# Optimization experiments

Hardware: AMD Instinct MI355X
Metric: run time of the kernel (lower is better)

Reference implementation:

```python
import jax, jax.numpy as jnp
import numpy as np

B, L, S, D, H, M, DFF, CO = 16, 512, 1024, 512, 8, 64, 2048, 512
KS = (3, 5, 7)  # MOEDecomp kernel sizes


def _avgpool(x, k):
    # AvgPool1d(kernel=k, stride=1, padding=k//2, count_include_pad=True) along L of [B,L,D]
    p = k // 2
    s = jax.lax.reduce_window(x, 0.0, jax.lax.add, (1, k, 1), (1, 1, 1), ((0, 0), (p, p), (0, 0)))
    return s / k


def _moe_decomp(x, w1, b1, w2, b2):
    trends = jnp.stack([_avgpool(x, k) for k in KS], axis=-1)          # [B,L,D,E]
    g = jax.nn.softmax(jax.nn.relu(x @ w1.T + b1) @ w2.T + b2, axis=-1)  # [B,L,E]
    trend = jnp.einsum('blde,ble->bld', trends, g)
    return x - trend, trend


def _fourier_block(x, wr, wi):
    b, l, d = x.shape
    qft = jnp.fft.rfft(x, axis=1)                                      # [B, L//2+1, D] complex
    m = min(M, qft.shape[1])
    W = wr[:, :, :m] + 1j * wi[:, :, :m]                               # [D,D,m] complex
    om = jnp.einsum('bmd,dem->bme', qft[:, :m], W)                     # per-mode complex matmul
    out_ft = jnp.zeros((b, l // 2 + 1, d), jnp.complex64).at[:, :m].set(om)
    return jnp.fft.irfft(out_ft, n=l, axis=1)


def _fourier_cross(q_in, kv, wq, bq, wk, bk, wv, bv, wo, bo):
    b, l, _ = q_in.shape
    s = kv.shape[1]
    dk = D // H
    q = (q_in @ wq.T + bq).reshape(b, l, H, dk).transpose(0, 2, 1, 3)   # [B,H,L,dk]
    k = (kv @ wk.T + bk).reshape(b, s, H, dk).transpose(0, 2, 1, 3)
    v = (kv @ wv.T + bv).reshape(b, s, H, dk).transpose(0, 2, 1, 3)
    qf = jnp.fft.rfft(q, axis=2)
    kf = jnp.fft.rfft(k, axis=2)
    vf = jnp.fft.rfft(v, axis=2)
    mq = min(M, qf.shape[2])
    mk = min(M, kf.shape[2])
    qf, kf, vf = qf[:, :, :mq], kf[:, :, :mk], vf[:, :, :mk]
    attn = (jnp.einsum('bhld,bhsd->bhls', qf.real, kf.real)
            + jnp.einsum('bhld,bhsd->bhls', qf.imag, kf.imag))
    attn = jax.nn.softmax(attn, axis=-1)
    of = jax.lax.complex(jnp.einsum('bhls,bhsd->bhld', attn, vf.real),
                         jnp.einsum('bhls,bhsd->bhld', attn, vf.imag))
    full = jnp.zeros((b, H, l // 2 + 1, dk), jnp.complex64).at[:, :, :mq].set(of)
    out = jnp.fft.irfft(full, n=l, axis=2)                              # [B,H,L,dk]
    out = out.transpose(0, 2, 1, 3).reshape(b, l, D)
    return out @ wo.T + bo


def _circ_conv(t, w):
    # Conv1d(k=3, padding=1, circular, no bias); t: [B,L,D], w: [CO,D,3]
    xt = t.transpose(0, 2, 1)                                           # [B,D,L]
    xp = jnp.concatenate([xt[:, :, -1:], xt, xt[:, :, :1]], axis=-1)
    y = jax.lax.conv_general_dilated(xp, w, (1,), 'VALID',
                                     dimension_numbers=('NCH', 'OIH', 'NCH'))
    return y.transpose(0, 2, 1)                                         # [B,L,CO]


def setup_inputs() -> dict:
    key = jax.random.key(0)
    ks = jax.random.split(key, 32)
    def n(i, shape, scale=0.02):
        return (scale * jax.random.normal(ks[i], shape)).astype(jnp.float32)
    feb_scale = 1.0 / (D * D)
    inp = {
        'x': n(0, (B, L, D), 1.0),
        'cross': n(1, (B, S, D), 1.0),
        'feb_wr': n(2, (D, D, M), feb_scale),
        'feb_wi': n(3, (D, D, M), feb_scale),
        'wq': n(4, (D, D)), 'bq': n(5, (D,)),
        'wk': n(6, (D, D)), 'bk': n(7, (D,)),
        'wv': n(8, (D, D)), 'bv': n(9, (D,)),
        'wo': n(10, (D, D)), 'bo': n(11, (D,)),
        'w_ff1': n(12, (DFF, D)), 'w_ff2': n(13, (D, DFF)),
        'd1_w1': n(14, (D // 2, D)), 'd1_b1': n(15, (D // 2,)),
        'd1_w2': n(16, (3, D // 2)), 'd1_b2': n(17, (3,)),
        'd2_w1': n(18, (D // 2, D)), 'd2_b1': n(19, (D // 2,)),
        'd2_w2': n(20, (3, D // 2)), 'd2_b2': n(21, (3,)),
        'd3_w1': n(22, (D // 2, D)), 'd3_b1': n(23, (D // 2,)),
        'd3_w2': n(24, (3, D // 2)), 'd3_b2': n(25, (3,)),
        'p1': n(26, (CO, D, 3)), 'p2': n(27, (CO, D, 3)), 'p3': n(28, (CO, D, 3)),
    }
    return inp


def reference(x, cross, feb_wr, feb_wi, wq, bq, wk, bk, wv, bv, wo, bo,
              w_ff1, w_ff2, d1_w1, d1_b1, d1_w2, d1_b2,
              d2_w1, d2_b1, d2_w2, d2_b2, d3_w1, d3_b1, d3_w2, d3_b2,
              p1, p2, p3):
    # dropout is identity (eval mode)
    x = x + _fourier_block(x, feb_wr, feb_wi)
    x, t1 = _moe_decomp(x, d1_w1, d1_b1, d1_w2, d1_b2)
    x = x + _fourier_cross(x, cross, wq, bq, wk, bk, wv, bv, wo, bo)
    x, t2 = _moe_decomp(x, d2_w1, d2_b1, d2_w2, d2_b2)
    y = jax.nn.relu(x @ w_ff1.T) @ w_ff2.T  # 1x1 convs == pointwise GEMMs
    x, t3 = _moe_decomp(x + y, d3_w1, d3_b1, d3_w2, d3_b2)
    residual_trend = _circ_conv(t1, p1) + _circ_conv(t2, p2) + _circ_conv(t3, p3)
    return x, residual_trend
```

## Files before the change

### kernel.cpp

```cpp
#include <hip/hip_runtime.h>
#include <math.h>

typedef unsigned short u16;
typedef unsigned int u32;
typedef unsigned long long u64;

constexpr int kB = 16, kL = 512, kS = 1024, kD = 512, kM = 64;

typedef __attribute__((ext_vector_type(8))) short u16x8;
typedef __attribute__((ext_vector_type(8))) _Float16 f16x8;
typedef __attribute__((ext_vector_type(4))) float f32x4;

__device__ __forceinline__ u16 f2h(float f) {
    _Float16 h = (_Float16)f;
    return *(u16*)&h;
}
__device__ __forceinline__ float h2f(u16 u) {
    _Float16 h = *(_Float16*)&u;
    return (float)h;
}

__global__ __launch_bounds__(256, 4) void gemm_fp16(
    const u16* __restrict__ Abase, const u16* __restrict__ Wbase,
    const float* __restrict__ bias, const float* __restrict__ resid,
    float* __restrict__ Cout, u16* __restrict__ Ch,
    int R, int N, int K, int flags,
    u64 zsA, u64 zsW, u64 zsC, u64 zsR, int lrsh)
{
    __shared__ __attribute__((aligned(16))) u16 Abuf[128 * 64];
    __shared__ __attribute__((aligned(16))) u16 Bbuf[128 * 64];
    const int zz = blockIdx.z;
    Abase += (u64)zz * zsA;
    Wbase += (u64)zz * zsW;
    if (Cout) Cout += (u64)zz * zsC;
    if (Ch)   Ch   += (u64)zz * zsC;
    if (resid) resid += (u64)zz * zsR;

    const int tid = threadIdx.x;
    const int lane = tid & 63;
    const int wave = tid >> 6;
    const int wr = wave >> 1, wc = wave & 1;
    const int ln15 = lane & 15, lq = lane >> 4;
    const int r0 = blockIdx.y * 128, n0 = blockIdx.x * 128;

    f32x4 acc[4][4];
#pragma unroll
    for (int m = 0; m < 4; ++m)
#pragma unroll
        for (int n = 0; n < 4; ++n) acc[m][n] = (f32x4){0.f, 0.f, 0.f, 0.f};

    for (int k0 = 0; k0 < K; k0 += 64) {
        u16x8 av[4], bv[4];
#pragma unroll
        for (int it = 0; it < 4; ++it) {
            int c = it * 256 + tid;
            int row = c >> 3, j = c & 7;
            int jj = j ^ (row & 7);
            av[it] = *(const u16x8*)(Abase + (size_t)(r0 + row) * K + k0 + jj * 8);
            bv[it] = *(const u16x8*)(Wbase + (size_t)(n0 + row) * K + k0 + jj * 8);
        }
        __syncthreads();
#pragma unroll
        for (int it = 0; it < 4; ++it) {
            int c = it * 256 + tid;
            int row = c >> 3, j = c & 7;
            *(u16x8*)&Abuf[row * 64 + j * 8] = av[it];
            *(u16x8*)&Bbuf[row * 64 + j * 8] = bv[it];
        }
        __syncthreads();
#pragma unroll
        for (int h = 0; h < 2; ++h) {
            int kg = lq + h * 4;
            f16x8 af[4], bfv[4];
#pragma unroll
            for (int m = 0; m < 4; ++m) {
                int row = wr * 64 + m * 16 + ln15;
                af[m] = *(const f16x8*)&Abuf[row * 64 + ((kg ^ (row & 7)) << 3)];
            }
#pragma unroll
            for (int n = 0; n < 4; ++n) {
                int col = wc * 64 + n * 16 + ln15;
                bfv[n] = *(const f16x8*)&Bbuf[col * 64 + ((kg ^ (col & 7)) << 3)];
            }
#pragma unroll
            for (int m = 0; m < 4; ++m)
#pragma unroll
                for (int n = 0; n < 4; ++n)
                    acc[m][n] = __builtin_amdgcn_mfma_f32_16x16x32_f16(af[m], bfv[n], acc[m][n], 0, 0, 0);
        }
        __syncthreads();
    }

#pragma unroll
    for (int m = 0; m < 4; ++m) {
#pragma unroll
        for (int n = 0; n < 4; ++n) {
            int gc = n0 + wc * 64 + n * 16 + ln15;
            float bv_ = bias ? bias[gc] : 0.f;
            int gr0 = r0 + wr * 64 + m * 16 + lq * 4;
            float v[4];
#pragma unroll
            for (int rg = 0; rg < 4; ++rg) {
                int gr = gr0 + rg;
                float val = acc[m][n][rg] + bv_;
                if (resid) val += resid[(size_t)gr * N + gc];
                if (flags & 1) val = fmaxf(val, 0.f);
                if (flags & 16) Cout[(size_t)gr * N + gc] = val;
                if (flags & 8)  Ch[(size_t)gr * N + gc] = f2h(val);
                v[rg] = val;
            }
            if (flags & 32) {
                int bb = gr0 >> lrsh;
                int l_ = gr0 & ((1 << lrsh) - 1);
                ushort4 o;
                o.x = f2h(v[0]); o.y = f2h(v[1]); o.z = f2h(v[2]); o.w = f2h(v[3]);
                *(ushort4*)&Ch[(((size_t)bb * N + gc) << lrsh) + l_] = o;
            }
        }
    }
}

__global__ __launch_bounds__(256, 4) void gemm64(
    const u16* __restrict__ Abase, const u16* __restrict__ Wbase,
    const float* __restrict__ bias, const float* __restrict__ resid,
    float* __restrict__ Cout, u16* __restrict__ Ch,
    int R, int N, int K, int flags,
    u64 zsA, u64 zsW, u64 zsC, u64 zsR, int lrsh)
{
    __shared__ __attribute__((aligned(16))) u16 Abuf[64 * 64];
    __shared__ __attribute__((aligned(16))) u16 Bbuf[64 * 64];
    const int zz = blockIdx.z;
    Abase += (u64)zz * zsA;
    Wbase += (u64)zz * zsW;
    if (Cout) Cout += (u64)zz * zsC;
    if (Ch)   Ch   += (u64)zz * zsC;
    if (resid) resid += (u64)zz * zsR;

    const int tid = threadIdx.x;
    const int lane = tid & 63;
    const int w = tid >> 6;
    const int ln15 = lane & 15, lq = lane >> 4;
    const int r0 = blockIdx.y * 64, n0 = blockIdx.x * 64;

    f32x4 acc[4];
#pragma unroll
    for (int m = 0; m < 4; ++m) acc[m] = (f32x4){0.f, 0.f, 0.f, 0.f};

    for (int k0 = 0; k0 < K; k0 += 64) {
        int t = 0, jsh = 0, dk = k0;
        if (flags & 4) {
            t = k0 / 1536;
            int rem = k0 - t * 1536;
            jsh = rem >> 9;
            dk = rem & 511;
        }
        u16x8 av[2], bv[2];
#pragma unroll
        for (int it = 0; it < 2; ++it) {
            int c = it * 256 + tid;
            int row = c >> 3, j = c & 7;
            int jj = j ^ (row & 7);
            size_t aoff, boff;
            if (flags & 4) {
                int grow = r0 + row;
                int b_ = grow >> 9, l_ = grow & 511;
                int sr = (b_ << 9) | ((l_ + jsh + 511) & 511);
                aoff = (size_t)t * (size_t)(kB * kL * kD) + (size_t)sr * 512 + dk + jj * 8;
                boff = (((size_t)(t * 3 + jsh) * 512) + n0 + row) * 512 + dk + jj * 8;
            } else {
                aoff = (size_t)(r0 + row) * K + k0 + jj * 8;
                boff = (size_t)(n0 + row) * K + k0 + jj * 8;
            }
            av[it] = *(const u16x8*)(Abase + aoff);
            bv[it] = *(const u16x8*)(Wbase + boff);
        }
        __syncthreads();
#pragma unroll
        for (int it = 0; it < 2; ++it) {
            int c = it * 256 + tid;
            int row = c >> 3, j = c & 7;
            *(u16x8*)&Abuf[row * 64 + j * 8] = av[it];
            *(u16x8*)&Bbuf[row * 64 + j * 8] = bv[it];
        }
        __syncthreads();
#pragma unroll
        for (int h = 0; h < 2; ++h) {
            int kg = lq + h * 4;
            int col = w * 16 + ln15;
            f16x8 bf = *(const f16x8*)&Bbuf[col * 64 + ((kg ^ (col & 7)) << 3)];
#pragma unroll
            for (int m = 0; m < 4; ++m) {
                int row = m * 16 + ln15;
                f16x8 af = *(const f16x8*)&Abuf[row * 64 + ((kg ^ (row & 7)) << 3)];
                acc[m] = __builtin_amdgcn_mfma_f32_16x16x32_f16(af, bf, acc[m], 0, 0, 0);
            }
        }
        __syncthreads();
    }

    const int gc = n0 + w * 16 + ln15;
    const float bv_ = bias ? bias[gc] : 0.f;
#pragma unroll
    for (int m = 0; m < 4; ++m) {
        int gr0 = r0 + m * 16 + lq * 4;
        float v[4];
#pragma unroll
        for (int rg = 0; rg < 4; ++rg) {
            int gr = gr0 + rg;
            float val = acc[m][rg] + bv_;
            if (resid) val += resid[(size_t)gr * N + gc];
            if (flags & 1) val = fmaxf(val, 0.f);
            if (flags & 16) Cout[(size_t)gr * N + gc] = val;
            if (flags & 8)  Ch[(size_t)gr * N + gc] = f2h(val);
            v[rg] = val;
        }
        if (flags & 32) {
            int bb = gr0 >> lrsh;
            int l_ = gr0 & ((1 << lrsh) - 1);
            ushort4 o;
            o.x = f2h(v[0]); o.y = f2h(v[1]); o.z = f2h(v[2]); o.w = f2h(v[3]);
            *(ushort4*)&Ch[(((size_t)bb * N + gc) << lrsh) + l_] = o;
        }
    }
}

__global__ __launch_bounds__(256) void prep(
    const float* __restrict__ wq, const float* __restrict__ wk,
    const float* __restrict__ wv, const float* __restrict__ wo,
    const float* __restrict__ ff1, const float* __restrict__ ff2,
    const float* __restrict__ dw1, const float* __restrict__ dw2,
    const float* __restrict__ dw3, const float* __restrict__ cross,
    const float* __restrict__ bk, const float* __restrict__ bv,
    u16* __restrict__ wqh, u16* __restrict__ wkvh, u16* __restrict__ woh,
    u16* __restrict__ ff1h, u16* __restrict__ ff2h,
    u16* __restrict__ d1w1h, u16* __restrict__ d2w1h, u16* __restrict__ d3w1h,
    u16* __restrict__ crossh, float* __restrict__ bkv,
    u16* __restrict__ tw512, u16* __restrict__ tw1024, u16* __restrict__ tih)
{
    const int gid = blockIdx.x * 256 + threadIdx.x;
    const int stride = gridDim.x * 256;
    for (int i = gid; i < 262144; i += stride) wqh[i] = f2h(wq[i]);
    for (int i = gid; i < 262144; i += stride) wkvh[i] = f2h(wk[i]);
    for (int i = gid; i < 262144; i += stride) wkvh[262144 + i] = f2h(wv[i]);
    for (int i = gid; i < 262144; i += stride) woh[i] = f2h(wo[i]);
    for (int i = gid; i < 1048576; i += stride) ff1h[i] = f2h(ff1[i]);
    for (int i = gid; i < 1048576; i += stride) ff2h[i] = f2h(ff2[i]);
    for (int i = gid; i < 131072; i += stride) d1w1h[i] = f2h(dw1[i]);
    for (int i = gid; i < 131072; i += stride) d2w1h[i] = f2h(dw2[i]);
    for (int i = gid; i < 131072; i += stride) d3w1h[i] = f2h(dw3[i]);
    const float4* c4 = (const float4*)cross;
    for (int i = gid; i < 2097152; i += stride) {
        float4 v = c4[i];
        ushort4 o;
        o.x = f2h(v.x); o.y = f2h(v.y); o.z = f2h(v.z); o.w = f2h(v.w);
        *(ushort4*)&crossh[i * 4] = o;
    }
    for (int i = gid; i < 1024; i += stride) bkv[i] = (i < 512) ? bk[i] : bv[i - 512];
    for (int i = gid; i < 65536; i += stride) {
        int r = i >> 9, l = i & 511;
        int m = r & 63;
        int ph = (m * l) & 511;
        float ang = 6.283185307179586f * (float)ph / 512.0f;
        float s_, c_;
        sincosf(ang, &s_, &c_);
        tw512[i] = f2h((r < 64) ? c_ : -s_);
    }
    for (int i = gid; i < 131072; i += stride) {
        int r = i >> 10, l = i & 1023;
        int m = r & 63;
        int ph = (m * l) & 1023;
        float ang = 6.283185307179586f * (float)ph / 1024.0f;
        float s_, c_;
        sincosf(ang, &s_, &c_);
        tw1024[i] = f2h((r < 64) ? c_ : -s_);
    }
    for (int i = gid; i < 65536; i += stride) {
        int l = i >> 7, r = i & 127;
        int m = r & 63;
        int ph = (m * l) & 511;
        float ang = 6.283185307179586f * (float)ph / 512.0f;
        float s_, c_;
        sincosf(ang, &s_, &c_);
        float val;
        if (r == 0) val = 1.0f / 512.0f;
        else if (r < 64) val = 2.0f * c_ / 512.0f;
        else if (r == 64) val = 0.0f;
        else val = -2.0f * s_ / 512.0f;
        tih[i] = f2h(val);
    }
}

__global__ __launch_bounds__(256) void repack_feb(
    const float* __restrict__ wr, const float* __restrict__ wi,
    u16* __restrict__ FW, u16* __restrict__ FI)
{
    __shared__ u16 t0[64][66], t1[64][66];
    const int e = blockIdx.x;
    const int d0 = blockIdx.y * 64;
    const int tid = threadIdx.x;
#pragma unroll
    for (int rep = 0; rep < 16; ++rep) {
        int idx = tid + rep * 256;
        int dd = idx >> 6, mm = idx & 63;
        size_t g = ((size_t)(d0 + dd) * 512 + e) * 64 + mm;
        t0[dd][mm] = f2h(wr[g]);
        t1[dd][mm] = f2h(wi[g]);
    }
    __syncthreads();
#pragma unroll
    for (int rep = 0; rep < 16; ++rep) {
        int idx = tid + rep * 256;
        int mm = idx >> 6, dd = idx & 63;
        size_t o = ((size_t)mm * 512 + e) * 512 + d0 + dd;
        FW[o] = t0[dd][mm];
        FI[o] = t1[dd][mm];
    }
}

__global__ __launch_bounds__(256, 4) void feb_mfma(
    const float* __restrict__ QF, const u16* __restrict__ FW,
    const u16* __restrict__ FI, u16* __restrict__ OMT)
{
    __shared__ __attribute__((aligned(16))) u16 Aq[16 * 64];
    __shared__ __attribute__((aligned(16))) u16 Ai[16 * 64];
    __shared__ __attribute__((aligned(16))) u16 Br[64 * 64];
    __shared__ __attribute__((aligned(16))) u16 Bi[64 * 64];
    const int e0 = blockIdx.x * 64;
    const int m  = blockIdx.y;
    const int tid = threadIdx.x;
    const int lane = tid & 63;
    const int w = tid >> 6;
    const int ln15 = lane & 15, lq = lane >> 4;

    f32x4 arr = (f32x4){0.f, 0.f, 0.f, 0.f};
    f32x4 aii = arr, ari = arr, air = arr;

    for (int d0 = 0; d0 < 512; d0 += 64) {
        u16x8 ahv;
        {
            int ar_ = tid >> 7;
            int row = (tid >> 3) & 15;
            int j = tid & 7;
            int jj = j ^ (row & 7);
            const float* src = QF + ((size_t)row * 128 + (ar_ ? 64 + m : m)) * 512 + d0 + jj * 8;
            float4 v0 = *(const float4*)src;
            float4 v1 = *(const float4*)(src + 4);
            ahv[0] = (short)f2h(v0.x); ahv[1] = (short)f2h(v0.y);
            ahv[2] = (short)f2h(v0.z); ahv[3] = (short)f2h(v0.w);
            ahv[4] = (short)f2h(v1.x); ahv[5] = (short)f2h(v1.y);
            ahv[6] = (short)f2h(v1.z); ahv[7] = (short)f2h(v1.w);
        }
        u16x8 bvv[4];
#pragma unroll
        for (int it = 0; it < 4; ++it) {
            int c = it * 256 + tid;
            int ar_ = c >> 9;
            int row = (c >> 3) & 63;
            int j = c & 7;
            int jj = j ^ (row & 7);
            const u16* src = (ar_ ? FI : FW) + ((size_t)m * 512 + e0 + row) * 512 + d0 + jj * 8;
            bvv[it] = *(const u16x8*)src;
        }
        __syncthreads();
        {
            int ar_ = tid >> 7;
            int row = (tid >> 3) & 15;
            int j = tid & 7;
            *(u16x8*)&((ar_ ? Ai : Aq)[row * 64 + j * 8]) = ahv;
        }
#pragma unroll
        for (int it = 0; it < 4; ++it) {
            int c = it * 256 + tid;
            int ar_ = c >> 9;
            int row = (c >> 3) & 63;
            int j = c & 7;
            *(u16x8*)&((ar_ ? Bi : Br)[row * 64 + j * 8]) = bvv[it];
        }
        __syncthreads();
#pragma unroll
        for (int h = 0; h < 2; ++h) {
            int kg = lq + h * 4;
            f16x8 aqf = *(const f16x8*)&Aq[ln15 * 64 + ((kg ^ (ln15 & 7)) << 3)];
            f16x8 aif = *(const f16x8*)&Ai[ln15 * 64 + ((kg ^ (ln15 & 7)) << 3)];
            int col = w * 16 + ln15;
            f16x8 brf = *(const f16x8*)&Br[col * 64 + ((kg ^ (col & 7)) << 3)];
            f16x8 bif = *(const f16x8*)&Bi[col * 64 + ((kg ^ (col & 7)) << 3)];
            arr = __builtin_amdgcn_mfma_f32_16x16x32_f16(aqf, brf, arr, 0, 0, 0);
            aii = __builtin_amdgcn_mfma_f32_16x16x32_f16(aif, bif, aii, 0, 0, 0);
            ari = __builtin_amdgcn_mfma_f32_16x16x32_f16(aqf, bif, ari, 0, 0, 0);
            air = __builtin_amdgcn_mfma_f32_16x16x32_f16(aif, brf, air, 0, 0, 0);
        }
        __syncthreads();
    }

    const int e = e0 + w * 16 + ln15;
#pragma unroll
    for (int rg = 0; rg < 4; ++rg) {
        int b = lq * 4 + rg;
        float omr = arr[rg] - aii[rg];
        float omi = ari[rg] + air[rg];
        u16* o = OMT + ((size_t)(b * 512 + e)) * 128;
        o[m] = f2h(omr);
        o[64 + m] = f2h(omi);
    }
}

__global__ __launch_bounds__(256) void tr_cast_x(
    const float* __restrict__ x, u16* __restrict__ xt)
{
    __shared__ u16 t[64][72];
    const int b = blockIdx.y;
    const int lt = (blockIdx.x >> 3) * 64, dt = (blockIdx.x & 7) * 64;
    const int tid = threadIdx.x;
#pragma unroll
    for (int rep = 0; rep < 16; ++rep) {
        int idx = tid + rep * 256;
        int row = idx >> 6, col = idx & 63;
        t[row][col] = f2h(x[((size_t)b * kL + lt + row) * kD + dt + col]);
    }
    __syncthreads();
#pragma unroll
    for (int rep = 0; rep < 16; ++rep) {
        int idx = tid + rep * 256;
        int row = idx >> 6, col = idx & 63;
        xt[((size_t)b * kD + dt + row) * kL + lt + col] = t[col][row];
    }
}

__global__ __launch_bounds__(256) void spectral_attn(
    const float* __restrict__ QF, const float* __restrict__ KVF,
    u16* __restrict__ OMT)
{
    __shared__ float kr[64][65], ki[64][65], sat[64][65];
    const int b = blockIdx.x >> 3, h = blockIdx.x & 7;
    const int tid = threadIdx.x;
    const int dbase = h * 64;
    const float* KVFb = KVF + (size_t)b * 128 * 1024;

    for (int idx = tid; idx < 4096; idx += 256) {
        int j = idx >> 6, dd = idx & 63;
        kr[j][dd] = KVFb[(size_t)j * 1024 + dbase + dd];
        ki[j][dd] = KVFb[(size_t)(64 + j) * 1024 + dbase + dd];
    }
    __syncthreads();

    const int i_ = tid >> 2, jg = tid & 3;
    float s[16];
#pragma unroll
    for (int jj = 0; jj < 16; ++jj) s[jj] = 0.f;
    const float* qrp = QF + ((size_t)b * 128 + i_) * 512 + dbase;
    const float* qip = qrp + (size_t)64 * 512;
    for (int dd = 0; dd < 64; ++dd) {
        float qr = qrp[dd], qi = qip[dd];
#pragma unroll
        for (int jj = 0; jj < 16; ++jj) {
            int j = jg * 16 + jj;
            s[jj] += qr * kr[j][dd] + qi * ki[j][dd];
        }
    }
    float mx = s[0];
#pragma unroll
    for (int jj = 1; jj < 16; ++jj) mx = fmaxf(mx, s[jj]);
    mx = fmaxf(mx, __shfl_xor(mx, 1));
    mx = fmaxf(mx, __shfl_xor(mx, 2));
    float sum = 0.f;
#pragma unroll
    for (int jj = 0; jj < 16; ++jj) { s[jj] = expf(s[jj] - mx); sum += s[jj]; }
    sum += __shfl_xor(sum, 1);
    sum += __shfl_xor(sum, 2);
    float rinv = 1.0f / sum;
#pragma unroll
    for (int jj = 0; jj < 16; ++jj) sat[i_][jg * 16 + jj] = s[jj] * rinv;
    __syncthreads();

    const int dd = tid & 63, ig = tid >> 6;
    float ar[16], ai[16];
#pragma unroll
    for (int ii = 0; ii < 16; ++ii) { ar[ii] = 0.f; ai[ii] = 0.f; }
    const float* VFb = KVFb + 512 + dbase + dd;
    for (int j = 0; j < 64; ++j) {
        float vr = VFb[(size_t)j * 1024];
        float vi = VFb[(size_t)(64 + j) * 1024];
#pragma unroll
        for (int ii = 0; ii < 16; ++ii) {
            float a = sat[ig * 16 + ii][j];
            ar[ii] += a * vr;
            ai[ii] += a * vi;
        }
    }
    u16* o = OMT + ((size_t)(b * 512 + dbase + dd)) * 128 + ig * 16;
    u16x8 v0, v1, w0, w1;
#pragma unroll
    for (int q = 0; q < 8; ++q) {
        v0[q] = (short)f2h(ar[q]);     v1[q] = (short)f2h(ar[8 + q]);
        w0[q] = (short)f2h(ai[q]);     w1[q] = (short)f2h(ai[8 + q]);
    }
    *(u16x8*)(o) = v0;
    *(u16x8*)(o + 8) = v1;
    *(u16x8*)(o + 64) = w0;
    *(u16x8*)(o + 72) = w1;
}

__global__ __launch_bounds__(256) void decomp_apply(
    const float* __restrict__ x, const float* __restrict__ logits,
    float* __restrict__ xout, u16* __restrict__ xout_h, u16* __restrict__ tout_h)
{
    int idx = blockIdx.x * 256 + threadIdx.x;
    if (idx >= kB * kL * kD) return;
    int d = idx & 511;
    int l = (idx >> 9) & 511;
    int b = idx >> 18;
    const float* lg = logits + ((size_t)b * kL + l) * 3;
    float g0 = lg[0], g1 = lg[1], g2 = lg[2];
    float m = fmaxf(g0, fmaxf(g1, g2));
    float e0 = expf(g0 - m), e1 = expf(g1 - m), e2 = expf(g2 - m);
    float inv = 1.0f / (e0 + e1 + e2);
    g0 = e0 * inv; g1 = e1 * inv; g2 = e2 * inv;

    const float* xb = x + (size_t)b * kL * kD + d;
    float v[7];
#pragma unroll
    for (int j = 0; j < 7; ++j) {
        int ls = l + j - 3;
        v[j] = (ls >= 0 && ls < kL) ? xb[(size_t)ls * kD] : 0.f;
    }
    float s3 = (v[2] + v[3] + v[4]) * (1.0f / 3.0f);
    float s5 = (v[1] + v[2] + v[3] + v[4] + v[5]) * 0.2f;
    float s7 = (v[0] + v[1] + v[2] + v[3] + v[4] + v[5] + v[6]) * (1.0f / 7.0f);
    float trend = g0 * s3 + g1 * s5 + g2 * s7;
    float res = v[3] - trend;
    if (xout) xout[idx] = res;
    if (xout_h) xout_h[idx] = f2h(res);
    tout_h[idx] = f2h(trend);
}

__global__ __launch_bounds__(256) void gate2(
    const u16* __restrict__ GH, const float* __restrict__ w2,
    const float* __restrict__ b2, float* __restrict__ logits)
{
    __shared__ float w2l[3][256];
    int tid = threadIdx.x;
    for (int i = tid; i < 768; i += 256) w2l[i >> 8][i & 255] = w2[i];
    __syncthreads();
    int gid = blockIdx.x * 256 + tid;
    int r = gid >> 2, q = gid & 3;
    float s0 = 0.f, s1 = 0.f, s2 = 0.f;
    const u16* g = GH + (size_t)r * 256 + q * 64;
    for (int c0 = 0; c0 < 64; c0 += 8) {
        uint4 u = *(const uint4*)&g[c0];
        u32 w[4] = {u.x, u.y, u.z, u.w};
#pragma unroll
        for (int p = 0; p < 4; ++p) {
            float f0 = h2f((u16)(w[p] & 0xFFFF));
            float f1 = h2f((u16)(w[p] >> 16));
            int c = q * 64 + c0 + p * 2;
            s0 += f0 * w2l[0][c] + f1 * w2l[0][c + 1];
            s1 += f0 * w2l[1][c] + f1 * w2l[1][c + 1];
            s2 += f0 * w2l[2][c] + f1 * w2l[2][c + 1];
        }
    }
    s0 += __shfl_xor(s0, 1); s0 += __shfl_xor(s0, 2);
    s1 += __shfl_xor(s1, 1); s1 += __shfl_xor(s1, 2);
    s2 += __shfl_xor(s2, 1); s2 += __shfl_xor(s2, 2);
    if (q == 0) {
        logits[(size_t)r * 3 + 0] = s0 + b2[0];
        logits[(size_t)r * 3 + 1] = s1 + b2[1];
        logits[(size_t)r * 3 + 2] = s2 + b2[2];
    }
}

__global__ void repack_p(const float* __restrict__ p1, const float* __restrict__ p2,
                         const float* __restrict__ p3, u16* __restrict__ pk)
{
    int idx = blockIdx.x * 256 + threadIdx.x;
    if (idx >= 3 * 3 * 512 * 512) return;
    int d = idx & 511;
    int oc = (idx >> 9) & 511;
    int j = (idx / (512 * 512)) % 3;
    int t = idx / (3 * 512 * 512);
    const float* p = (t == 0) ? p1 : (t == 1) ? p2 : p3;
    pk[idx] = f2h(p[(size_t)oc * 512 * 3 + (size_t)d * 3 + j]);
}

extern "C" void kernel_launch(void* const* d_in, const int* in_sizes, int n_in,
                              void* d_out, int out_size, void* d_ws, size_t ws_size,
                              hipStream_t stream)
{
    const float* x_in   = (const float*)d_in[0];
    const float* cross  = (const float*)d_in[1];
    const float* feb_wr = (const float*)d_in[2];
    const float* feb_wi = (const float*)d_in[3];
    const float* wq = (const float*)d_in[4];
    const float* bq = (const float*)d_in[5];
    const float* wk = (const float*)d_in[6];
    const float* bk = (const float*)d_in[7];
    const float* wv = (const float*)d_in[8];
    const float* bv = (const float*)d_in[9];
    const float* wo = (const float*)d_in[10];
    const float* bo = (const float*)d_in[11];
    const float* w_ff1 = (const float*)d_in[12];
    const float* w_ff2 = (const float*)d_in[13];
    const float* d1_w1 = (const float*)d_in[14];
    const float* d1_b1 = (const float*)d_in[15];
    const float* d1_w2 = (const float*)d_in[16];
    const float* d1_b2 = (const float*)d_in[17];
    const float* d2_w1 = (const float*)d_in[18];
    const float* d2_b1 = (const float*)d_in[19];
    const float* d2_w2 = (const float*)d_in[20];
    const float* d2_b2 = (const float*)d_in[21];
    const float* d3_w1 = (const float*)d_in[22];
    const float* d3_b1 = (const float*)d_in[23];
    const float* d3_w2 = (const float*)d_in[24];
    const float* d3_b2 = (const float*)d_in[25];
    const float* p1 = (const float*)d_in[26];
    const float* p2 = (const float*)d_in[27];
    const float* p3 = (const float*)d_in[28];

    float* ws = (float*)d_ws;
    float* X    = ws;
    float* XT   = ws + 4194304;
    u16*  KVt   = (u16*)(ws + 8388608);
    u16*  Q0t   = (u16*)(ws + 16777216);
    u16*  T1h   = (u16*)(ws + 18874368);
    u16*  T2h   = (u16*)(ws + 20971520);
    u16*  T3h   = (u16*)(ws + 23068672);
    float* QF   = ws + 25165824;
    float* KVF  = ws + 26214400;
    u16*  OMTh  = (u16*)(ws + 28311552);
    u16*  crossh = (u16*)(ws + 29884416);
    u16*  Xh    = (u16*)(ws + 34078720);
    u16*  XTh   = (u16*)(ws + 36175872);
    u16*  GHh   = (u16*)(ws + 38273024);
    float* GLG  = ws + 39321600;
    u16*  wqh   = (u16*)(ws + 39346176);
    u16*  wkvh  = wqh + 262144;
    u16*  woh   = wkvh + 524288;
    u16*  ff1h  = woh + 262144;
    u16*  ff2h  = ff1h + 1048576;
    u16*  d1w1h = ff2h + 1048576;
    u16*  d2w1h = d1w1h + 131072;
    u16*  d3w1h = d2w1h + 131072;
    u16*  PKh   = d3w1h + 131072;
    u16*  TW512h  = (u16*)(ws + 42295296);
    u16*  TW1024h = (u16*)(ws + 42328064);
    u16*  TIh     = (u16*)(ws + 42393600);
    float* bkv    = ws + 42426368;
    u16*  FWh   = (u16*)X;
    u16*  FIh   = (u16*)KVt;
    u16*  xTh   = Q0t;
    u16*  HIDh  = KVt;
    u16*  Qh    = Q0t;

    float* outx = (float*)d_out;
    float* outt = outx + 4194304;

    auto g128 = [&](const u16* A, const u16* W, const float* bias, const float* resid,
                    float* C, u16* Cb, int R, int N, int K, int flags,
                    int Z, u64 zsA, u64 zsW, u64 zsC, u64 zsR, int lrsh) {
        dim3 g(N / 128, R / 128, Z);
        hipLaunchKernelGGL(gemm_fp16, g, dim3(256), 0, stream,
                           A, W, bias, resid, C, Cb, R, N, K, flags, zsA, zsW, zsC, zsR, lrsh);
    };
    auto g64 = [&](const u16* A, const u16* W, const float* bias, const float* resid,
                   float* C, u16* Cb, int R, int N, int K, int flags,
                   int Z, u64 zsA, u64 zsW, u64 zsC, u64 zsR, int lrsh) {
        dim3 g(N / 64, R / 64, Z);
        hipLaunchKernelGGL(gemm64, g, dim3(256), 0, stream,
                           A, W, bias, resid, C, Cb, R, N, K, flags, zsA, zsW, zsC, zsR, lrsh);
    };

    hipLaunchKernelGGL(prep, dim3(2048), dim3(256), 0, stream,
                       wq, wk, wv, wo, w_ff1, w_ff2, d1_w1, d2_w1, d3_w1, cross, bk, bv,
                       wqh, wkvh, woh, ff1h, ff2h, d1w1h, d2w1h, d3w1h, crossh, bkv,
                       TW512h, TW1024h, TIh);
    hipLaunchKernelGGL(repack_p, dim3(9216), dim3(256), 0, stream, p1, p2, p3, PKh);
    hipLaunchKernelGGL(repack_feb, dim3(512, 8), dim3(256), 0, stream,
                       feb_wr, feb_wi, FWh, FIh);

    hipLaunchKernelGGL(tr_cast_x, dim3(64, 16), dim3(256), 0, stream, x_in, xTh);
    g64(TW512h, xTh, nullptr, nullptr, QF, nullptr, 128, 512, 512, 16,
        16, 0, (u64)512 * 512, (u64)128 * 512, 0, 0);
    hipLaunchKernelGGL(feb_mfma, dim3(8, 64), dim3(256), 0, stream, QF, FWh, FIh, OMTh);
    g64(TIh, OMTh, nullptr, x_in, X, Xh, 512, 512, 128, 16 | 8,
        16, 0, (u64)512 * 128, (u64)512 * 512, (u64)512 * 512, 0);

    g64(Xh, d1w1h, d1_b1, nullptr, nullptr, GHh, 8192, 256, 512, 1 | 8, 1, 0, 0, 0, 0, 0);
    hipLaunchKernelGGL(gate2, dim3(128), dim3(256), 0, stream, GHh, d1_w2, d1_b2, GLG);
    hipLaunchKernelGGL(decomp_apply, dim3(16384), dim3(256), 0, stream, X, GLG, XT, XTh, T1h);

    g64(XTh, wqh, bq, nullptr, nullptr, Q0t, 8192, 512, 512, 32, 1, 0, 0, 0, 0, 9);
    g128(crossh, wkvh, bkv, nullptr, nullptr, KVt, 16384, 1024, 512, 32, 1, 0, 0, 0, 0, 10);
    g64(TW512h, Q0t, nullptr, nullptr, QF, nullptr, 128, 512, 512, 16,
        16, 0, (u64)512 * 512, (u64)128 * 512, 0, 0);
    g64(TW1024h, KVt, nullptr, nullptr, KVF, nullptr, 128, 1024, 1024, 16,
        16, 0, (u64)1024 * 1024, (u64)128 * 1024, 0, 0);
    hipLaunchKernelGGL(spectral_attn, dim3(128), dim3(256), 0, stream, QF, KVF, OMTh);
    g64(TIh, OMTh, nullptr, nullptr, nullptr, Qh, 512, 512, 128, 8,
        16, 0, (u64)512 * 128, (u64)512 * 512, 0, 0);
    g64(Qh, woh, bo, XT, X, Xh, 8192, 512, 512, 16 | 8, 1, 0, 0, 0, 0, 0);

    g64(Xh, d2w1h, d2_b1, nullptr, nullptr, GHh, 8192, 256, 512, 1 | 8, 1, 0, 0, 0, 0, 0);
    hipLaunchKernelGGL(gate2, dim3(128), dim3(256), 0, stream, GHh, d2_w2, d2_b2, GLG);
    hipLaunchKernelGGL(decomp_apply, dim3(16384), dim3(256), 0, stream, X, GLG, XT, XTh, T2h);

    g128(XTh, ff1h, nullptr, nullptr, nullptr, HIDh, 8192, 2048, 512, 1 | 8, 1, 0, 0, 0, 0, 0);
    g64(HIDh, ff2h, nullptr, XT, X, Xh, 8192, 512, 2048, 16 | 8, 1, 0, 0, 0, 0, 0);

    g64(Xh, d3w1h, d3_b1, nullptr, nullptr, GHh, 8192, 256, 512, 1 | 8, 1, 0, 0, 0, 0, 0);
    hipLaunchKernelGGL(gate2, dim3(128), dim3(256), 0, stream, GHh, d3_w2, d3_b2, GLG);
    hipLaunchKernelGGL(decomp_apply, dim3(16384), dim3(256), 0, stream, X, GLG, outx,
                       (u16*)nullptr, T3h);

    g64(T1h, PKh, nullptr, nullptr, outt, nullptr, 8192, 512, 4608, 4 | 16,
        1, 0, 0, 0, 0, 0);

    (void)in_sizes; (void)n_in; (void)out_size; (void)ws_size;
}
```

Baseline: 526.0 us.

## Split circular-conv GEMM into three shift slices on 128-tile kernel plus reduction

```diff
diff --git a/kernel.cpp b/kernel.cpp
--- a/kernel.cpp
+++ b/kernel.cpp
@@ -50,14 +50,31 @@
         for (int n = 0; n < 4; ++n) acc[m][n] = (f32x4){0.f, 0.f, 0.f, 0.f};
 
     for (int k0 = 0; k0 < K; k0 += 64) {
+        int t = 0, jsh = 0, dk = k0;
+        if (flags & 4) {
+            t = k0 >> 9;
+            jsh = zz;
+            dk = k0 & 511;
+        }
         u16x8 av[4], bv[4];
 #pragma unroll
         for (int it = 0; it < 4; ++it) {
             int c = it * 256 + tid;
             int row = c >> 3, j = c & 7;
             int jj = j ^ (row & 7);
-            av[it] = *(const u16x8*)(Abase + (size_t)(r0 + row) * K + k0 + jj * 8);
-            bv[it] = *(const u16x8*)(Wbase + (size_t)(n0 + row) * K + k0 + jj * 8);
+            size_t aoff, boff;
+            if (flags & 4) {
+                int grow = r0 + row;
+                int b_ = grow >> 9, l_ = grow & 511;
+                int sr = (b_ << 9) | ((l_ + jsh + 511) & 511);
+                aoff = (size_t)t * (size_t)(kB * kL * kD) + (size_t)sr * 512 + dk + jj * 8;
+                boff = (((size_t)(t * 3 + jsh) * 512) + n0 + row) * 512 + dk + jj * 8;
+            } else {
+                aoff = (size_t)(r0 + row) * K + k0 + jj * 8;
+                boff = (size_t)(n0 + row) * K + k0 + jj * 8;
+            }
+            av[it] = *(const u16x8*)(Abase + aoff);
+            bv[it] = *(const u16x8*)(Wbase + boff);
         }
         __syncthreads();
 #pragma unroll
@@ -147,32 +164,14 @@
     for (int m = 0; m < 4; ++m) acc[m] = (f32x4){0.f, 0.f, 0.f, 0.f};
 
     for (int k0 = 0; k0 < K; k0 += 64) {
-        int t = 0, jsh = 0, dk = k0;
-        if (flags & 4) {
-            t = k0 / 1536;
-            int rem = k0 - t * 1536;
-            jsh = rem >> 9;
-            dk = rem & 511;
-        }
         u16x8 av[2], bv[2];
 #pragma unroll
         for (int it = 0; it < 2; ++it) {
             int c = it * 256 + tid;
             int row = c >> 3, j = c & 7;
             int jj = j ^ (row & 7);
-            size_t aoff, boff;
-            if (flags & 4) {
-                int grow = r0 + row;
-                int b_ = grow >> 9, l_ = grow & 511;
-                int sr = (b_ << 9) | ((l_ + jsh + 511) & 511);
-                aoff = (size_t)t * (size_t)(kB * kL * kD) + (size_t)sr * 512 + dk + jj * 8;
-                boff = (((size_t)(t * 3 + jsh) * 512) + n0 + row) * 512 + dk + jj * 8;
-            } else {
-                aoff = (size_t)(r0 + row) * K + k0 + jj * 8;
-                boff = (size_t)(n0 + row) * K + k0 + jj * 8;
-            }
-            av[it] = *(const u16x8*)(Abase + aoff);
-            bv[it] = *(const u16x8*)(Wbase + boff);
+            av[it] = *(const u16x8*)(Abase + (size_t)(r0 + row) * K + k0 + jj * 8);
+            bv[it] = *(const u16x8*)(Wbase + (size_t)(n0 + row) * K + k0 + jj * 8);
         }
         __syncthreads();
 #pragma unroll
@@ -580,6 +579,26 @@
     int t = idx / (3 * 512 * 512);
     const float* p = (t == 0) ? p1 : (t == 1) ? p2 : p3;
     pk[idx] = f2h(p[(size_t)oc * 512 * 3 + (size_t)d * 3 + j]);
+}
+
+__global__ __launch_bounds__(256) void conv_sum2(
+    const u16* __restrict__ Cc, float* __restrict__ outt)
+{
+    int gid = blockIdx.x * 256 + threadIdx.x;
+    size_t base = (size_t)gid * 8;
+    float s[8];
+#pragma unroll
+    for (int q = 0; q < 8; ++q) s[q] = 0.f;
+#pragma unroll
+    for (int j = 0; j < 3; ++j) {
+        const u16x8 v = *(const u16x8*)&Cc[(size_t)j * 8192 * 512 + base];
+#pragma unroll
+        for (int q = 0; q < 8; ++q) s[q] += h2f((u16)v[q]);
+    }
+    float4 o0 = {s[0], s[1], s[2], s[3]};
+    float4 o1 = {s[4], s[5], s[6], s[7]};
+    *(float4*)&outt[base] = o0;
+    *(float4*)&outt[base + 4] = o1;
 }
 
 extern "C" void kernel_launch(void* const* d_in, const int* in_sizes, int n_in,
@@ -650,6 +669,7 @@
     u16*  xTh   = Q0t;
     u16*  HIDh  = KVt;
     u16*  Qh    = Q0t;
+    u16*  Cch   = (u16*)ws;
 
     float* outx = (float*)d_out;
     float* outt = outx + 4194304;
@@ -711,8 +731,9 @@
     hipLaunchKernelGGL(decomp_apply, dim3(16384), dim3(256), 0, stream, X, GLG, outx,
                        (u16*)nullptr, T3h);
 
-    g64(T1h, PKh, nullptr, nullptr, outt, nullptr, 8192, 512, 4608, 4 | 16,
-        1, 0, 0, 0, 0, 0);
+    g128(T1h, PKh, nullptr, nullptr, nullptr, Cch, 8192, 512, 1536, 4 | 8,
+         3, 0, 0, (u64)8192 * 512, 0, 0);
+    hipLaunchKernelGGL(conv_sum2, dim3(2048), dim3(256), 0, stream, Cch, outt);
 
     (void)in_sizes; (void)n_in; (void)out_size; (void)ws_size;
 }
```

Result: faster. 503.7 us (-4.2%).
